# Kernel optimization log

Hardware: AMD Instinct MI355X
Metric: run time of the kernel (lower is better)

## Reference

```python
import jax, jax.numpy as jnp
import numpy as np

B, T, DIN, H = 32, 4096, 256, 256


def _log_g(x):
    # log of g(x) = where(x>=0, x+0.5, sigmoid(x)), computed stably in log space
    return jnp.where(x >= 0.0, jnp.log(jax.nn.relu(x) + 0.5), -jax.nn.softplus(-x))


def setup_inputs() -> dict:
    key = jax.random.key(0)
    ks = jax.random.split(key, 4)
    scale = (6.0 / (DIN + H)) ** 0.5  # xavier_uniform
    return {
        "x": jax.random.normal(ks[0], (B, T, DIN), dtype=jnp.float32),
        "h0": jax.random.normal(ks[1], (B, 1, H), dtype=jnp.float32),
        "Wz": jax.random.uniform(ks[2], (H, DIN), jnp.float32, -scale, scale),
        "bz": jnp.zeros((H,), jnp.float32),
        "Wh": jax.random.uniform(ks[3], (H, DIN), jnp.float32, -scale, scale),
        "bh": jnp.zeros((H,), jnp.float32),
    }


def reference(x, h0, Wz, bz, Wh, bh):
    # minGRU training path: log-space parallel scan (Heinsen scan)
    k = jnp.einsum("bti,hi->bth", x, Wz) + bz            # pre-activation of z gate
    log_z = -jax.nn.softplus(-k)                           # log sigmoid(k)
    log_coeffs = -jax.nn.softplus(k)                       # log(1 - sigmoid(k))
    log_h0 = _log_g(h0)                                    # (B,1,H)
    log_tilde_h = _log_g(jnp.einsum("bti,hi->bth", x, Wh) + bh)
    log_values = jnp.concatenate([log_h0, log_z + log_tilde_h], axis=1)  # (B,T+1,H)
    # a_star[t] = sum_{s<=t} log_coeffs[s], with a leading zero
    a_star = jnp.cumsum(jnp.pad(log_coeffs, ((0, 0), (1, 0), (0, 0))), axis=1)
    # logcumsumexp along time via associative scan with logaddexp
    lcse = jax.lax.associative_scan(jnp.logaddexp, log_values - a_star, axis=1)
    log_h = a_star + lcse                                  # (B,T+1,H)
    return jnp.exp(log_h[:, 1:])                           # (B,T,H)
```

## Files before the change

### kernel.cpp

```cpp
#include <hip/hip_runtime.h>
#include <hip/hip_fp16.h>

typedef __attribute__((ext_vector_type(8))) short short8;
typedef __attribute__((ext_vector_type(4))) float f32x4;
typedef unsigned short ushort_t;
typedef unsigned int uint_t;

#define B_SZ 32
#define T_SZ 4096
#define D_IN 256
#define H_SZ 256
#define M_SZ (B_SZ * T_SZ)
#define CHUNK 64
#define NCHUNK (T_SZ / CHUNK)

__device__ __forceinline__ ushort_t f2bf(float f) {
  unsigned int u = __float_as_uint(f);
  unsigned int r = (u + 0x7FFFu + ((u >> 16) & 1u)) >> 16;
  return (ushort_t)r;
}

__device__ __forceinline__ float sigmoidf_(float xv) {
  float e = __expf(-fabsf(xv));
  float s = 1.0f / (1.0f + e);
  return xv >= 0.0f ? s : 1.0f - s;
}

__device__ __forceinline__ float unpack_lo(uint_t pk) {
  return __half2float(__ushort_as_half((ushort_t)(pk & 0xFFFFu)));
}
__device__ __forceinline__ float unpack_hi(uint_t pk) {
  return __half2float(__ushort_as_half((ushort_t)(pk >> 16)));
}

__global__ void prep_w(const float* __restrict__ Wz, const float* __restrict__ Wh,
                       ushort_t* __restrict__ wsB) {
  int g = blockIdx.x * 256 + threadIdx.x;
  if (g >= 8 * 2048) return;
  int ks = g >> 11;
  int gi = g & 2047;
  int n = gi >> 2;
  int cs = gi & 3;
  int c = cs ^ (n & 3);
  int h = (n >> 5) * 16 + (n & 15);
  const float* W = ((n >> 4) & 1) ? Wh : Wz;
  const float* src = W + (size_t)h * D_IN + ks * 32 + c * 8;
  ushort_t* dst = wsB + (size_t)g * 8;
#pragma unroll
  for (int j = 0; j < 8; ++j) dst[j] = f2bf(src[j]);
  (void)ks;
}

__global__ __launch_bounds__(512, 2) void gemm_av(
    const float* __restrict__ x, const ushort_t* __restrict__ wsB,
    const float* __restrict__ bz, const float* __restrict__ bh,
    uint_t* __restrict__ av) {
  __shared__ __align__(16) unsigned char lds[81920];
  ushort_t* As = (ushort_t*)lds;
  ushort_t* Bs = (ushort_t*)(lds + 16384);

  const int tid = threadIdx.x;
  const int lane = tid & 63;
  const int wid = tid >> 6;
  const int wr = wid >> 2;
  const int wc = wid & 3;
  const int m0 = blockIdx.x * 128;

  const int arow = tid >> 2;
  const int ac = tid & 3;
  const int agran = arow * 4 + (ac ^ (arow & 3));
  const float* asrc = x + (size_t)(m0 + arow) * D_IN + ac * 8;

  f32x4 acc[4][8];
#pragma unroll
  for (int rt = 0; rt < 4; ++rt)
#pragma unroll
    for (int ct = 0; ct < 8; ++ct) {
      f32x4 z4 = {0.f, 0.f, 0.f, 0.f};
      acc[rt][ct] = z4;
    }

  {
    const ushort_t* bsrc = wsB + 0 * 16384 + wid * 2048 + lane * 8;
    ushort_t* bdst = Bs + 0 * 16384 + wid * 2048;
#pragma unroll
    for (int cc = 0; cc < 4; ++cc) {
      __builtin_amdgcn_global_load_lds(
          (const __attribute__((address_space(1))) void*)(bsrc + cc * 512),
          (__attribute__((address_space(3))) void*)(bdst + cc * 512), 16, 0, 0);
    }
    float4 f0 = *(const float4*)(asrc);
    float4 f1 = *(const float4*)(asrc + 4);
    short8 vfr;
    ushort_t* vp = (ushort_t*)&vfr;
    vp[0] = f2bf(f0.x); vp[1] = f2bf(f0.y); vp[2] = f2bf(f0.z); vp[3] = f2bf(f0.w);
    vp[4] = f2bf(f1.x); vp[5] = f2bf(f1.y); vp[6] = f2bf(f1.z); vp[7] = f2bf(f1.w);
    *(short8*)(As + agran * 8) = vfr;
  }
  __syncthreads();

#pragma unroll
  for (int ks = 0; ks < 8; ++ks) {
    const int cur = ks & 1;
    short8 afr[4], bfr[8];
#pragma unroll
    for (int rt = 0; rt < 4; ++rt) {
      int row = wr * 64 + rt * 16 + (lane & 15);
      int gran = row * 4 + ((lane >> 4) ^ (row & 3));
      afr[rt] = *(const short8*)(As + cur * 4096 + gran * 8);
    }
#pragma unroll
    for (int ct = 0; ct < 8; ++ct) {
      int n = wc * 128 + ct * 16 + (lane & 15);
      int gran = n * 4 + ((lane >> 4) ^ (n & 3));
      bfr[ct] = *(const short8*)(Bs + cur * 16384 + gran * 8);
    }
    float4 nf0, nf1;
    if (ks < 7) {
      const ushort_t* bsrc = wsB + (size_t)(ks + 1) * 16384 + wid * 2048 + lane * 8;
      ushort_t* bdst = Bs + (cur ^ 1) * 16384 + wid * 2048;
#pragma unroll
      for (int cc = 0; cc < 4; ++cc) {
        __builtin_amdgcn_global_load_lds(
            (const __attribute__((address_space(1))) void*)(bsrc + cc * 512),
            (__attribute__((address_space(3))) void*)(bdst + cc * 512), 16, 0, 0);
      }
      nf0 = *(const float4*)(asrc + (ks + 1) * 32);
      nf1 = *(const float4*)(asrc + (ks + 1) * 32 + 4);
    }
#pragma unroll
    for (int rt = 0; rt < 4; ++rt)
#pragma unroll
      for (int ct = 0; ct < 8; ++ct)
        acc[rt][ct] = __builtin_amdgcn_mfma_f32_16x16x32_bf16(
            afr[rt], bfr[ct], acc[rt][ct], 0, 0, 0);
    if (ks < 7) {
      short8 vfr;
      ushort_t* vp = (ushort_t*)&vfr;
      vp[0] = f2bf(nf0.x); vp[1] = f2bf(nf0.y); vp[2] = f2bf(nf0.z); vp[3] = f2bf(nf0.w);
      vp[4] = f2bf(nf1.x); vp[5] = f2bf(nf1.y); vp[6] = f2bf(nf1.z); vp[7] = f2bf(nf1.w);
      *(short8*)(As + (cur ^ 1) * 4096 + agran * 8) = vfr;
    }
    __syncthreads();
  }

  const int col16 = lane & 15;
  const int rgrp = lane >> 4;
#pragma unroll
  for (int i = 0; i < 4; ++i) {
    int hh = (wc * 4 + i) * 16 + col16;
    float bzv = bz[hh];
    float bhv = bh[hh];
#pragma unroll
    for (int rt = 0; rt < 4; ++rt) {
#pragma unroll
      for (int j = 0; j < 4; ++j) {
        int row = m0 + wr * 64 + rt * 16 + rgrp * 4 + j;
        float kv = acc[rt][2 * i][j] + bzv;
        float pv = acc[rt][2 * i + 1][j] + bhv;
        float a = sigmoidf_(-kv);
        float z = 1.0f - a;
        float gg = (pv >= 0.0f) ? (pv + 0.5f) : sigmoidf_(pv);
        float vv = z * gg;
        uint_t pk = (uint_t)__half_as_ushort(__float2half_rn(a)) |
                    ((uint_t)__half_as_ushort(__float2half_rn(vv)) << 16);
        av[(size_t)row * H_SZ + hh] = pk;
      }
    }
  }
}

__global__ __launch_bounds__(256) void chunk_reduce(
    const uint_t* __restrict__ av, float2* __restrict__ cAV) {
  const int b = blockIdx.x >> 6;
  const int c = blockIdx.x & 63;
  const int h = threadIdx.x;
  const uint_t* p = av + ((size_t)b * T_SZ + c * CHUNK) * H_SZ + h;

  uint_t buf[CHUNK];
#pragma unroll
  for (int s = 0; s < CHUNK; ++s) buf[s] = p[(size_t)s * H_SZ];

  float A = 1.0f, V = 0.0f;
#pragma unroll
  for (int s = 0; s < CHUNK; ++s) {
    float a = unpack_lo(buf[s]);
    float v = unpack_hi(buf[s]);
    A = a * A;
    V = fmaf(a, V, v);
  }
  float2 r; r.x = A; r.y = V;
  cAV[((size_t)b * NCHUNK + c) * H_SZ + h] = r;
}

__global__ __launch_bounds__(256) void chunk_carry(
    const float* __restrict__ h0, const float2* __restrict__ cAV,
    float* __restrict__ hb) {
  const int b = blockIdx.x;
  const int h = threadIdx.x;
  float v0 = h0[b * H_SZ + h];
  float hc = (v0 >= 0.0f) ? (v0 + 0.5f) : sigmoidf_(v0);

  const float2* p = cAV + (size_t)b * NCHUNK * H_SZ + h;
  float* o = hb + (size_t)b * NCHUNK * H_SZ + h;

  float2 buf[NCHUNK];
#pragma unroll
  for (int c = 0; c < NCHUNK; ++c) buf[c] = p[(size_t)c * H_SZ];

#pragma unroll
  for (int c = 0; c < NCHUNK; ++c) {
    o[(size_t)c * H_SZ] = hc;
    hc = fmaf(buf[c].x, hc, buf[c].y);
  }
}

__global__ __launch_bounds__(256) void chunk_scan_out(
    const uint_t* av, const float* __restrict__ hb, float* out) {
  const int b = blockIdx.x >> 6;
  const int c = blockIdx.x & 63;
  const int h = threadIdx.x;

  float hc = hb[((size_t)b * NCHUNK + c) * H_SZ + h];
  const uint_t* p = av + ((size_t)b * T_SZ + c * CHUNK) * H_SZ + h;
  float* o = out + ((size_t)b * T_SZ + c * CHUNK) * H_SZ + h;

  uint_t buf[CHUNK];
#pragma unroll
  for (int s = 0; s < CHUNK; ++s) buf[s] = p[(size_t)s * H_SZ];

#pragma unroll
  for (int s = 0; s < CHUNK; ++s) {
    float a = unpack_lo(buf[s]);
    float v = unpack_hi(buf[s]);
    hc = fmaf(a, hc, v);
    o[(size_t)s * H_SZ] = hc;
  }
}

__global__ __launch_bounds__(64) void scan_seq(const float* __restrict__ h0,
                                               const uint_t* av, float* out) {
  const int b = blockIdx.x >> 2;
  const int hg = blockIdx.x & 3;
  const int h = hg * 64 + threadIdx.x;

  float v0 = h0[b * H_SZ + h];
  float hc = (v0 >= 0.0f) ? (v0 + 0.5f) : sigmoidf_(v0);

  const uint_t* p = av + (size_t)b * T_SZ * H_SZ + h;
  float* o = out + (size_t)b * T_SZ * H_SZ + h;

  uint_t buf[32];
#pragma unroll
  for (int d = 0; d < 32; ++d) buf[d] = p[(size_t)d * H_SZ];

  for (int t0 = 0; t0 < T_SZ; t0 += 32) {
#pragma unroll
    for (int d = 0; d < 32; ++d) {
      int t = t0 + d;
      uint_t pk = buf[d];
      int tn = t + 32;
      if (tn < T_SZ) buf[d] = p[(size_t)tn * H_SZ];
      hc = fmaf(unpack_lo(pk), hc, unpack_hi(pk));
      o[(size_t)t * H_SZ] = hc;
    }
  }
}

extern "C" void kernel_launch(void* const* d_in, const int* in_sizes, int n_in,
                              void* d_out, int out_size, void* d_ws, size_t ws_size,
                              hipStream_t stream) {
  const float* x  = (const float*)d_in[0];
  const float* h0 = (const float*)d_in[1];
  const float* Wz = (const float*)d_in[2];
  const float* bz = (const float*)d_in[3];
  const float* Wh = (const float*)d_in[4];
  const float* bh = (const float*)d_in[5];
  float* out = (float*)d_out;

  const size_t wsBBytes = 262144;
  const size_t cavBytes = (size_t)B_SZ * NCHUNK * H_SZ * 8;
  const size_t hbBytes  = (size_t)B_SZ * NCHUNK * H_SZ * 4;
  const size_t avOff    = 8388608;
  const size_t avBytes  = (size_t)M_SZ * H_SZ * 4;

  ushort_t* wsB = (ushort_t*)d_ws;
  float2* cAV = (float2*)((char*)d_ws + wsBBytes);
  float* hb   = (float*)((char*)d_ws + wsBBytes + cavBytes);

  const bool haveSummaries = ws_size >= wsBBytes + cavBytes + hbBytes;
  uint_t* av;
  if (ws_size >= avOff + avBytes) {
    av = (uint_t*)((char*)d_ws + avOff);
  } else {
    av = (uint_t*)d_out;
  }

  prep_w<<<64, 256, 0, stream>>>(Wz, Wh, wsB);
  gemm_av<<<M_SZ / 128, 512, 0, stream>>>(x, wsB, bz, bh, av);
  if (haveSummaries) {
    chunk_reduce<<<B_SZ * NCHUNK, 256, 0, stream>>>(av, cAV);
    chunk_carry<<<B_SZ, 256, 0, stream>>>(h0, cAV, hb);
    chunk_scan_out<<<B_SZ * NCHUNK, 256, 0, stream>>>(av, hb, out);
  } else {
    scan_seq<<<B_SZ * 4, 64, 0, stream>>>(h0, av, out);
  }
}
```

Before: 182.2 us.

## Shrink GEMM M-tile to 64 rows with all warps split along N

The fused GEMM tile drops from 128 to 64 rows. All 8 warps now split the 512-wide N dimension, so each warp holds 4x4 accumulators instead of 4x8. The weight and activation LDS layouts change from XOR-swizzled to column-major granule ordering, and the launch bound asks for 4 blocks per CU to cut register and LDS pressure and raise occupancy. In exchange, weight tiles are reloaded twice as often per output row, only half the threads load A, and dropping the swizzle may bring LDS bank conflicts.

```diff
diff --git a/kernel.cpp b/kernel.cpp
--- a/kernel.cpp
+++ b/kernel.cpp
@@ -38,82 +38,81 @@
   int g = blockIdx.x * 256 + threadIdx.x;
   if (g >= 8 * 2048) return;
   int ks = g >> 11;
-  int gi = g & 2047;
-  int n = gi >> 2;
-  int cs = gi & 3;
-  int c = cs ^ (n & 3);
+  int r = g & 2047;
+  int c = r >> 9;
+  int n = r & 511;
   int h = (n >> 5) * 16 + (n & 15);
   const float* W = ((n >> 4) & 1) ? Wh : Wz;
   const float* src = W + (size_t)h * D_IN + ks * 32 + c * 8;
   ushort_t* dst = wsB + (size_t)g * 8;
 #pragma unroll
   for (int j = 0; j < 8; ++j) dst[j] = f2bf(src[j]);
-  (void)ks;
-}
-
-__global__ __launch_bounds__(512, 2) void gemm_av(
+}
+
+__global__ __launch_bounds__(512, 4) void gemm_av(
     const float* __restrict__ x, const ushort_t* __restrict__ wsB,
     const float* __restrict__ bz, const float* __restrict__ bh,
     uint_t* __restrict__ av) {
-  __shared__ __align__(16) unsigned char lds[81920];
+  __shared__ __align__(16) unsigned char lds[73728];
   ushort_t* As = (ushort_t*)lds;
-  ushort_t* Bs = (ushort_t*)(lds + 16384);
+  ushort_t* Bs = (ushort_t*)(lds + 8192);
 
   const int tid = threadIdx.x;
   const int lane = tid & 63;
   const int wid = tid >> 6;
-  const int wr = wid >> 2;
-  const int wc = wid & 3;
-  const int m0 = blockIdx.x * 128;
-
-  const int arow = tid >> 2;
-  const int ac = tid & 3;
-  const int agran = arow * 4 + (ac ^ (arow & 3));
-  const float* asrc = x + (size_t)(m0 + arow) * D_IN + ac * 8;
-
-  f32x4 acc[4][8];
+  const int m0 = blockIdx.x * 64;
+
+  const int a_row = tid & 63;
+  const int a_g = tid >> 6;
+  const float* asrc = x + (size_t)(m0 + a_row) * D_IN + a_g * 8;
+
+  f32x4 acc[4][4];
 #pragma unroll
   for (int rt = 0; rt < 4; ++rt)
 #pragma unroll
-    for (int ct = 0; ct < 8; ++ct) {
+    for (int ct = 0; ct < 4; ++ct) {
       f32x4 z4 = {0.f, 0.f, 0.f, 0.f};
       acc[rt][ct] = z4;
     }
 
   {
-    const ushort_t* bsrc = wsB + 0 * 16384 + wid * 2048 + lane * 8;
-    ushort_t* bdst = Bs + 0 * 16384 + wid * 2048;
+    const ushort_t* bsrc = wsB + (size_t)wid * 2048 + lane * 8;
+    ushort_t* bdst = Bs + wid * 2048;
 #pragma unroll
     for (int cc = 0; cc < 4; ++cc) {
       __builtin_amdgcn_global_load_lds(
           (const __attribute__((address_space(1))) void*)(bsrc + cc * 512),
           (__attribute__((address_space(3))) void*)(bdst + cc * 512), 16, 0, 0);
     }
-    float4 f0 = *(const float4*)(asrc);
-    float4 f1 = *(const float4*)(asrc + 4);
-    short8 vfr;
-    ushort_t* vp = (ushort_t*)&vfr;
-    vp[0] = f2bf(f0.x); vp[1] = f2bf(f0.y); vp[2] = f2bf(f0.z); vp[3] = f2bf(f0.w);
-    vp[4] = f2bf(f1.x); vp[5] = f2bf(f1.y); vp[6] = f2bf(f1.z); vp[7] = f2bf(f1.w);
-    *(short8*)(As + agran * 8) = vfr;
+    if (tid < 256) {
+      float4 f0 = *(const float4*)(asrc);
+      float4 f1 = *(const float4*)(asrc + 4);
+      short8 vfr;
+      ushort_t* vp = (ushort_t*)&vfr;
+      vp[0] = f2bf(f0.x); vp[1] = f2bf(f0.y); vp[2] = f2bf(f0.z); vp[3] = f2bf(f0.w);
+      vp[4] = f2bf(f1.x); vp[5] = f2bf(f1.y); vp[6] = f2bf(f1.z); vp[7] = f2bf(f1.w);
+      *(short8*)(As + tid * 8) = vfr;
+    }
   }
   __syncthreads();
 
 #pragma unroll
   for (int ks = 0; ks < 8; ++ks) {
     const int cur = ks & 1;
-    short8 afr[4], bfr[8];
-#pragma unroll
-    for (int rt = 0; rt < 4; ++rt) {
-      int row = wr * 64 + rt * 16 + (lane & 15);
-      int gran = row * 4 + ((lane >> 4) ^ (row & 3));
-      afr[rt] = *(const short8*)(As + cur * 4096 + gran * 8);
-    }
-#pragma unroll
-    for (int ct = 0; ct < 8; ++ct) {
-      int n = wc * 128 + ct * 16 + (lane & 15);
-      int gran = n * 4 + ((lane >> 4) ^ (n & 3));
-      bfr[ct] = *(const short8*)(Bs + cur * 16384 + gran * 8);
+    short8 afr[4], bfr[4];
+    {
+      const int c = lane >> 4;
+      const int r16 = lane & 15;
+#pragma unroll
+      for (int rt = 0; rt < 4; ++rt) {
+        int row = rt * 16 + r16;
+        afr[rt] = *(const short8*)(As + cur * 2048 + (c * 64 + row) * 8);
+      }
+#pragma unroll
+      for (int ct = 0; ct < 4; ++ct) {
+        int n = wid * 64 + ct * 16 + r16;
+        bfr[ct] = *(const short8*)(Bs + cur * 16384 + (c * 512 + n) * 8);
+      }
     }
     float4 nf0, nf1;
     if (ks < 7) {
@@ -125,21 +124,23 @@
             (const __attribute__((address_space(1))) void*)(bsrc + cc * 512),
             (__attribute__((address_space(3))) void*)(bdst + cc * 512), 16, 0, 0);
       }
-      nf0 = *(const float4*)(asrc + (ks + 1) * 32);
-      nf1 = *(const float4*)(asrc + (ks + 1) * 32 + 4);
+      if (tid < 256) {
+        nf0 = *(const float4*)(asrc + (ks + 1) * 32);
+        nf1 = *(const float4*)(asrc + (ks + 1) * 32 + 4);
+      }
     }
 #pragma unroll
     for (int rt = 0; rt < 4; ++rt)
 #pragma unroll
-      for (int ct = 0; ct < 8; ++ct)
+      for (int ct = 0; ct < 4; ++ct)
         acc[rt][ct] = __builtin_amdgcn_mfma_f32_16x16x32_bf16(
             afr[rt], bfr[ct], acc[rt][ct], 0, 0, 0);
-    if (ks < 7) {
+    if (ks < 7 && tid < 256) {
       short8 vfr;
       ushort_t* vp = (ushort_t*)&vfr;
       vp[0] = f2bf(nf0.x); vp[1] = f2bf(nf0.y); vp[2] = f2bf(nf0.z); vp[3] = f2bf(nf0.w);
       vp[4] = f2bf(nf1.x); vp[5] = f2bf(nf1.y); vp[6] = f2bf(nf1.z); vp[7] = f2bf(nf1.w);
-      *(short8*)(As + (cur ^ 1) * 4096 + agran * 8) = vfr;
+      *(short8*)(As + (cur ^ 1) * 2048 + tid * 8) = vfr;
     }
     __syncthreads();
   }
@@ -147,15 +148,15 @@
   const int col16 = lane & 15;
   const int rgrp = lane >> 4;
 #pragma unroll
-  for (int i = 0; i < 4; ++i) {
-    int hh = (wc * 4 + i) * 16 + col16;
+  for (int i = 0; i < 2; ++i) {
+    int hh = (wid * 2 + i) * 16 + col16;
     float bzv = bz[hh];
     float bhv = bh[hh];
 #pragma unroll
     for (int rt = 0; rt < 4; ++rt) {
 #pragma unroll
       for (int j = 0; j < 4; ++j) {
-        int row = m0 + wr * 64 + rt * 16 + rgrp * 4 + j;
+        int row = m0 + rt * 16 + rgrp * 4 + j;
         float kv = acc[rt][2 * i][j] + bzv;
         float pv = acc[rt][2 * i + 1][j] + bhv;
         float a = sigmoidf_(-kv);
@@ -297,7 +298,7 @@
   }
 
   prep_w<<<64, 256, 0, stream>>>(Wz, Wh, wsB);
-  gemm_av<<<M_SZ / 128, 512, 0, stream>>>(x, wsB, bz, bh, av);
+  gemm_av<<<M_SZ / 64, 512, 0, stream>>>(x, wsB, bz, bh, av);
   if (haveSummaries) {
     chunk_reduce<<<B_SZ * NCHUNK, 256, 0, stream>>>(av, cAV);
     chunk_carry<<<B_SZ, 256, 0, stream>>>(h0, cAV, hb);
```

After: 174.7 us. 1.04x faster.
